# Kernel tuning notes

Hardware: AMD Instinct MI355X
Metric: run time of the kernel (lower is better)

Reference implementation:

```python
import jax, jax.numpy as jnp
import numpy as np


def setup_inputs() -> dict:
    key = jax.random.key(0)
    k1, k2, k3, k4, k5 = jax.random.split(key, 5)
    B, S, H, V = 16, 256, 1024, 32000
    std = 0.02
    return {
        "input_ids": jax.random.randint(k1, (B, S), 0, V, dtype=jnp.int64),
        "emb": jax.random.normal(k2, (V, H), dtype=jnp.float32) * std,
        "w_hx": jax.random.normal(k3, (H, H), dtype=jnp.float32) * std,
        "w_hh": jax.random.normal(k4, (H, H), dtype=jnp.float32) * std,
        "w_yh": jax.random.normal(k5, (V, H), dtype=jnp.float32) * std,
    }


def reference(input_ids, emb, w_hx, w_hh, w_yh):
    # input_ids: [B, S] int; emb: [V, H]; w_*: torch Linear weights [out, in]
    B, S = input_ids.shape
    H = emb.shape[1]
    x = emb[input_ids]                         # [B, S, H]
    # Precompute input contribution for all timesteps: x_t @ w_hx.T
    xin = jnp.einsum('bsh,oh->bso', x, w_hx)   # [B, S, H]
    h0 = jnp.zeros((B, H), dtype=x.dtype)

    def step(h, xin_t):
        h_new = jnp.tanh(xin_t + h @ w_hh.T)   # [B, H]
        return h_new, h_new

    _, hs = jax.lax.scan(step, h0, jnp.swapaxes(xin, 0, 1))  # hs: [S, B, H]
    hs = jnp.swapaxes(hs, 0, 1)                # [B, S, H]
    logits = jnp.einsum('bsh,vh->bsv', hs, w_yh)  # [B, S, V]
    return logits
```

## Files before the change

kernel.cpp:

```cpp
#include <hip/hip_runtime.h>
#include <stdint.h>

typedef __attribute__((ext_vector_type(8)))  short   short8;
typedef __attribute__((ext_vector_type(8)))  unsigned short ushort8;
typedef __attribute__((ext_vector_type(8)))  __bf16  bf16x8;
typedef __attribute__((ext_vector_type(4)))  float   floatx4;
typedef __attribute__((ext_vector_type(4)))  unsigned short ushort4v;

#define AS1 __attribute__((address_space(1)))
#define AS3 __attribute__((address_space(3)))

__device__ __forceinline__ unsigned short f2bf(float f) {
  unsigned u = __builtin_bit_cast(unsigned, f);
  u = (u + 0x7FFFu + ((u >> 16) & 1u)) >> 16;
  return (unsigned short)u;
}
__device__ __forceinline__ float bf2f(unsigned short h) {
  unsigned u = ((unsigned)h) << 16;
  return __builtin_bit_cast(float, u);
}

__global__ __launch_bounds__(256) void convert_bf16(const float* __restrict__ src,
                                                    unsigned short* __restrict__ dst,
                                                    int n) {
  int i = (blockIdx.x * 256 + threadIdx.x) * 4;
  if (i >= n) return;
  float4 v = *(const float4*)(src + i);
  ushort4v o;
  o.x = f2bf(v.x); o.y = f2bf(v.y); o.z = f2bf(v.z); o.w = f2bf(v.w);
  *(ushort4v*)(dst + i) = o;
}

__global__ __launch_bounds__(256) void detect_i64(const int* __restrict__ idbuf,
                                                  int* __restrict__ flag) {
  int v = 0;
  for (int i = threadIdx.x; i < 2048; i += 256) v |= idbuf[2 * i + 1];
  if (v != 0) atomicOr(flag, 1);
}

__global__ __launch_bounds__(256) void gather_embed(const int* __restrict__ ids,
                                                    const float* __restrict__ emb,
                                                    unsigned short* __restrict__ xbf,
                                                    const int* __restrict__ flag) {
  int i = blockIdx.x;
  int row = (*flag != 0) ? ids[i] : ids[2 * i];
  const float* src = emb + (size_t)row * 1024 + threadIdx.x * 4;
  float4 v = *(const float4*)src;
  ushort4v o;
  o.x = f2bf(v.x); o.y = f2bf(v.y); o.z = f2bf(v.z); o.w = f2bf(v.w);
  *(ushort4v*)(xbf + (size_t)i * 1024 + threadIdx.x * 4) = o;
}

__global__ __launch_bounds__(256) void gemm_bt(const unsigned short* __restrict__ A,
                                               const unsigned short* __restrict__ B,
                                               float* __restrict__ C,
                                               int M, int N, int K) {
  __shared__ unsigned short lA[128 * 64];
  __shared__ unsigned short lB[128 * 64];
  const int nwg  = gridDim.x;
  const int wgid = blockIdx.x;
  const int q    = nwg >> 3;
  const int swz  = (wgid & 7) * q + (wgid >> 3);
  const int ntx  = N >> 7;
  const int bx   = swz % ntx;
  const int by   = swz / ntx;
  const int tid  = threadIdx.x;
  const int lane = tid & 63;
  const int w    = tid >> 6;
  const int wr   = w >> 1, wc = w & 1;

  floatx4 acc[4][4];
#pragma unroll
  for (int m = 0; m < 4; ++m)
#pragma unroll
    for (int n = 0; n < 4; ++n) acc[m][n] = (floatx4){0.f, 0.f, 0.f, 0.f};

  const size_t rowA0 = (size_t)by * 128;
  const size_t colB0 = (size_t)bx * 128;

  for (int k0 = 0; k0 < K; k0 += 64) {
#pragma unroll
    for (int p = 0; p < 4; ++p) {
      int cc = p * 256 + tid;
      int r  = cc >> 3;
      int c8 = cc & 7;
      const unsigned short* srcA = A + (rowA0 + r) * K + k0 + c8 * 8;
      const unsigned short* srcB = B + (colB0 + r) * K + k0 + c8 * 8;
      __builtin_amdgcn_global_load_lds((const AS1 unsigned int*)srcA,
                                       (AS3 unsigned int*)&lA[cc * 8], 16, 0, 0);
      __builtin_amdgcn_global_load_lds((const AS1 unsigned int*)srcB,
                                       (AS3 unsigned int*)&lB[cc * 8], 16, 0, 0);
    }
    __syncthreads();
#pragma unroll
    for (int kk = 0; kk < 2; ++kk) {
      const int kofs = kk * 32 + (lane >> 4) * 8;
      bf16x8 af[4], bfv[4];
#pragma unroll
      for (int m = 0; m < 4; ++m) {
        int r = wr * 64 + m * 16 + (lane & 15);
        af[m] = *(const bf16x8*)&lA[r * 64 + kofs];
      }
#pragma unroll
      for (int n = 0; n < 4; ++n) {
        int r = wc * 64 + n * 16 + (lane & 15);
        bfv[n] = *(const bf16x8*)&lB[r * 64 + kofs];
      }
#pragma unroll
      for (int m = 0; m < 4; ++m)
#pragma unroll
        for (int n = 0; n < 4; ++n)
          acc[m][n] = __builtin_amdgcn_mfma_f32_16x16x32_bf16(af[m], bfv[n], acc[m][n], 0, 0, 0);
    }
    __syncthreads();
  }

#pragma unroll
  for (int m = 0; m < 4; ++m) {
#pragma unroll
    for (int j = 0; j < 4; ++j) {
      size_t row = rowA0 + wr * 64 + m * 16 + ((lane >> 4) * 4 + j);
      float* crow = C + row * (size_t)N + colB0 + wc * 64 + (lane & 15);
#pragma unroll
      for (int n = 0; n < 4; ++n) crow[n * 16] = acc[m][n][j];
    }
  }
}

__global__ __launch_bounds__(1024, 4) void rnn_step_all(const float* __restrict__ xin,
                                                        const unsigned short* __restrict__ whh_bf,
                                                        float* __restrict__ hs,
                                                        unsigned short* __restrict__ hs_bf) {
  const int b     = blockIdx.x >> 4;
  const int slice = blockIdx.x & 15;
  const int tid   = threadIdx.x;
  const int o     = tid & 63;
  const int kc    = tid >> 6;

  __shared__ __align__(16) float hl[1024];
  __shared__ float red[2][1024];

  float wf[64];
  {
    const unsigned short* wrow = whh_bf + (size_t)(slice * 64 + o) * 1024 + kc * 64;
#pragma unroll
    for (int j = 0; j < 8; ++j) {
      ushort8 wv = *(const ushort8*)(wrow + j * 8);
#pragma unroll
      for (int e = 0; e < 8; ++e) wf[j * 8 + e] = bf2f(wv[e]);
    }
#pragma unroll
    for (int j = 0; j < 64; ++j) asm volatile("" : "+v"(wf[j]));
  }

  const size_t bbase = (size_t)b * 256 * 1024;

  for (int t = 0; t < 256; ++t) {
    float s = 0.0f;
    if (tid < 64) s = xin[bbase + (size_t)t * 1024 + slice * 64 + tid];

    if (t == 0) {
      hl[tid] = 0.0f;
    } else {
      const float* src = &hs[bbase + (size_t)(t - 1) * 1024 + (size_t)kc * 64 + o];
      float v;
      do {
        v = __hip_atomic_load(src, __ATOMIC_RELAXED, __HIP_MEMORY_SCOPE_AGENT);
      } while (__any(v != v));
      hl[tid] = v;
    }

    float sum = 0.0f;
#pragma unroll
    for (int j4 = 0; j4 < 16; ++j4) {
      float4 hv = *(const float4*)&hl[kc * 64 + j4 * 4];
      sum += wf[j4 * 4 + 0] * hv.x + wf[j4 * 4 + 1] * hv.y +
             wf[j4 * 4 + 2] * hv.z + wf[j4 * 4 + 3] * hv.w;
    }
    red[t & 1][tid] = sum;
    __syncthreads();

    if (tid < 64) {
#pragma unroll
      for (int k2 = 0; k2 < 16; ++k2) s += red[t & 1][k2 * 64 + tid];
      float e  = __expf(2.0f * s);
      float hv = 1.0f - 2.0f * __builtin_amdgcn_rcpf(e + 1.0f);
      size_t idx = bbase + (size_t)t * 1024 + (size_t)slice * 64 + tid;
      __hip_atomic_store(&hs[idx], hv, __ATOMIC_RELAXED, __HIP_MEMORY_SCOPE_AGENT);
      hs_bf[idx] = f2bf(hv);
    }
  }
}

extern "C" void kernel_launch(void* const* d_in, const int* in_sizes, int n_in,
                              void* d_out, int out_size, void* d_ws, size_t ws_size,
                              hipStream_t stream) {
  const int*   ids  = (const int*)d_in[0];
  const float* emb  = (const float*)d_in[1];
  const float* w_hx = (const float*)d_in[2];
  const float* w_hh = (const float*)d_in[3];
  const float* w_yh = (const float*)d_in[4];
  float*       out  = (float*)d_out;

  const int B = 16, S = 256, H = 1024, V = 32000;
  const int BS = B * S;

  char*  ws  = (char*)d_ws;
  size_t off = 0;
  auto alloc = [&](size_t bytes) {
    size_t cur = off;
    off += (bytes + 255) & ~(size_t)255;
    return (void*)(ws + cur);
  };

  unsigned short* whx_bf = (unsigned short*)alloc((size_t)H * H * 2);
  unsigned short* whh_bf = (unsigned short*)alloc((size_t)H * H * 2);
  unsigned short* wyh_bf = (unsigned short*)alloc((size_t)V * H * 2);
  unsigned short* x_bf   = (unsigned short*)alloc((size_t)BS * H * 2);
  float*          xin    = (float*)alloc((size_t)BS * H * 4);
  float*          hs     = (float*)alloc((size_t)BS * H * 4);
  unsigned short* hs_bf  = (unsigned short*)alloc((size_t)BS * H * 2);
  int*            dflag  = (int*)alloc(256);

  hipMemsetAsync(hs, 0xFF, (size_t)BS * H * 4, stream);
  hipMemsetAsync(dflag, 0, 256, stream);

  detect_i64<<<dim3(1), dim3(256), 0, stream>>>(ids, dflag);
  convert_bf16<<<dim3((H * H) / 1024), dim3(256), 0, stream>>>(w_hx, whx_bf, H * H);
  convert_bf16<<<dim3((H * H) / 1024), dim3(256), 0, stream>>>(w_hh, whh_bf, H * H);
  convert_bf16<<<dim3((V * H) / 1024), dim3(256), 0, stream>>>(w_yh, wyh_bf, V * H);
  gather_embed<<<dim3(BS), dim3(256), 0, stream>>>(ids, emb, x_bf, dflag);

  gemm_bt<<<dim3((BS / 128) * (H / 128)), dim3(256), 0, stream>>>(x_bf, whx_bf, xin, BS, H, H);

  rnn_step_all<<<dim3(256), dim3(1024), 0, stream>>>(xin, whh_bf, hs, hs_bf);

  gemm_bt<<<dim3((BS / 128) * (V / 128)), dim3(256), 0, stream>>>(hs_bf, wyh_bf, out, BS, V, H);
}
```

Baseline: 931.9 us.

## Halve RNN block size and replace __syncthreads with LDS flag handoff

The recurrent step kernel now uses 512 threads per block, each holding 128 weights in registers instead of 64, which halves the cross-wave reduction. The per-step __syncthreads is replaced by per-wave LDS flags that only the reducing wave spins on, so the other waves can move on to poll the next timestep. This aims to cut barrier and reduction latency on the serial critical path. In exchange it doubles per-thread register use, and it relies on hand-placed waitcnt and sched_barrier ordering for correctness, which could race if the compiler reorders memory operations.

New measurement: 977.9 us. 1.05x slower.

```diff
diff --git a/kernel.cpp b/kernel.cpp
--- a/kernel.cpp
+++ b/kernel.cpp
@@ -127,10 +127,10 @@
   }
 }
 
-__global__ __launch_bounds__(1024, 4) void rnn_step_all(const float* __restrict__ xin,
-                                                        const unsigned short* __restrict__ whh_bf,
-                                                        float* __restrict__ hs,
-                                                        unsigned short* __restrict__ hs_bf) {
+__global__ __launch_bounds__(512, 2) void rnn_step_all(const float* __restrict__ xin,
+                                                       const unsigned short* __restrict__ whh_bf,
+                                                       float* __restrict__ hs,
+                                                       unsigned short* __restrict__ hs_bf) {
   const int b     = blockIdx.x >> 4;
   const int slice = blockIdx.x & 15;
   const int tid   = threadIdx.x;
@@ -138,54 +138,72 @@
   const int kc    = tid >> 6;
 
   __shared__ __align__(16) float hl[1024];
-  __shared__ float red[2][1024];
-
-  float wf[64];
+  __shared__ float red[2][512];
+  __shared__ unsigned lflag[2][8];
+
+  if (tid < 16) lflag[tid >> 3][tid & 7] = 0;
+  __syncthreads();
+
+  float wf[128];
   {
-    const unsigned short* wrow = whh_bf + (size_t)(slice * 64 + o) * 1024 + kc * 64;
-#pragma unroll
-    for (int j = 0; j < 8; ++j) {
+    const unsigned short* wrow = whh_bf + (size_t)(slice * 64 + o) * 1024 + kc * 128;
+#pragma unroll
+    for (int j = 0; j < 16; ++j) {
       ushort8 wv = *(const ushort8*)(wrow + j * 8);
 #pragma unroll
       for (int e = 0; e < 8; ++e) wf[j * 8 + e] = bf2f(wv[e]);
     }
 #pragma unroll
-    for (int j = 0; j < 64; ++j) asm volatile("" : "+v"(wf[j]));
+    for (int j = 0; j < 128; ++j) asm volatile("" : "+v"(wf[j]));
   }
 
   const size_t bbase = (size_t)b * 256 * 1024;
 
   for (int t = 0; t < 256; ++t) {
     float s = 0.0f;
-    if (tid < 64) s = xin[bbase + (size_t)t * 1024 + slice * 64 + tid];
+    if (tid < 64) s = xin[bbase + (size_t)t * 1024 + slice * 64 + o];
 
     if (t == 0) {
-      hl[tid] = 0.0f;
+      hl[kc * 128 + o]      = 0.0f;
+      hl[kc * 128 + 64 + o] = 0.0f;
     } else {
-      const float* src = &hs[bbase + (size_t)(t - 1) * 1024 + (size_t)kc * 64 + o];
-      float v;
+      const float* src = &hs[bbase + (size_t)(t - 1) * 1024 + (size_t)kc * 128];
+      float v1, v2;
       do {
-        v = __hip_atomic_load(src, __ATOMIC_RELAXED, __HIP_MEMORY_SCOPE_AGENT);
-      } while (__any(v != v));
-      hl[tid] = v;
-    }
-
-    float sum = 0.0f;
-#pragma unroll
-    for (int j4 = 0; j4 < 16; ++j4) {
-      float4 hv = *(const float4*)&hl[kc * 64 + j4 * 4];
-      sum += wf[j4 * 4 + 0] * hv.x + wf[j4 * 4 + 1] * hv.y +
-             wf[j4 * 4 + 2] * hv.z + wf[j4 * 4 + 3] * hv.w;
-    }
-    red[t & 1][tid] = sum;
-    __syncthreads();
+        v1 = __hip_atomic_load(src + o,      __ATOMIC_RELAXED, __HIP_MEMORY_SCOPE_AGENT);
+        v2 = __hip_atomic_load(src + 64 + o, __ATOMIC_RELAXED, __HIP_MEMORY_SCOPE_AGENT);
+      } while (__any((v1 != v1) | (v2 != v2)));
+      hl[kc * 128 + o]      = v1;
+      hl[kc * 128 + 64 + o] = v2;
+    }
+
+    float a0 = 0.f, a1 = 0.f, a2 = 0.f, a3 = 0.f;
+#pragma unroll
+    for (int j4 = 0; j4 < 32; ++j4) {
+      float4 hv = *(const float4*)&hl[kc * 128 + j4 * 4];
+      a0 += wf[j4 * 4 + 0] * hv.x; a1 += wf[j4 * 4 + 1] * hv.y;
+      a2 += wf[j4 * 4 + 2] * hv.z; a3 += wf[j4 * 4 + 3] * hv.w;
+    }
+    red[t & 1][tid] = (a0 + a1) + (a2 + a3);
+    asm volatile("s_waitcnt lgkmcnt(0)" ::: "memory");
+    __builtin_amdgcn_sched_barrier(0);
+    if (o == 0) lflag[t & 1][kc] = (unsigned)(t + 1);
 
     if (tid < 64) {
-#pragma unroll
-      for (int k2 = 0; k2 < 16; ++k2) s += red[t & 1][k2 * 64 + tid];
+      const volatile unsigned* fl = &lflag[t & 1][0];
+      bool rdy;
+      do {
+        rdy = true;
+#pragma unroll
+        for (int k = 0; k < 8; ++k) rdy = rdy && (fl[k] >= (unsigned)(t + 1));
+      } while (!rdy);
+      __builtin_amdgcn_sched_barrier(0);
+      asm volatile("" ::: "memory");
+#pragma unroll
+      for (int k2 = 0; k2 < 8; ++k2) s += red[t & 1][k2 * 64 + o];
       float e  = __expf(2.0f * s);
       float hv = 1.0f - 2.0f * __builtin_amdgcn_rcpf(e + 1.0f);
-      size_t idx = bbase + (size_t)t * 1024 + (size_t)slice * 64 + tid;
+      size_t idx = bbase + (size_t)t * 1024 + (size_t)slice * 64 + o;
       __hip_atomic_store(&hs[idx], hv, __ATOMIC_RELAXED, __HIP_MEMORY_SCOPE_AGENT);
       hs_bf[idx] = f2bf(hv);
     }
@@ -233,7 +251,7 @@
 
   gemm_bt<<<dim3((BS / 128) * (H / 128)), dim3(256), 0, stream>>>(x_bf, whx_bf, xin, BS, H, H);
 
-  rnn_step_all<<<dim3(256), dim3(1024), 0, stream>>>(xin, whh_bf, hs, hs_bf);
+  rnn_step_all<<<dim3(256), dim3(512), 0, stream>>>(xin, whh_bf, hs, hs_bf);
 
   gemm_bt<<<dim3((BS / 128) * (V / 128)), dim3(256), 0, stream>>>(hs_bf, wyh_bf, out, BS, V, H);
 }
```

## Replace per-batch scalar RNN recurrence with MFMA wavefronts over all batches

Applied to the files above, without the earlier changes.

The recurrent step moves from 256 blocks of 1024 threads (one per batch-slice) doing scalar FMAs with LDS reductions to 64 single-wave blocks. Each block owns 16 output neurons across all 16 batches and computes h@W_hh^T with bf16 MFMA, keeping its weights in registers. The hidden state now lives only in a time-major bf16 buffer that is polled with NaN sentinels, replacing the separate fp32 and bf16 copies. The GEMMs gain a row remap so xin is written time-major and logits are read back into batch-major order. This cuts per-step sync and reduction overhead and memory traffic, at the cost of bf16 rounding of the recurrent state and busy-wait spins on fewer waves.

Measured after the change: 1.845 ms. 98.0% more time.

```diff
diff --git a/kernel.cpp b/kernel.cpp
--- a/kernel.cpp
+++ b/kernel.cpp
@@ -14,10 +14,6 @@
   unsigned u = __builtin_bit_cast(unsigned, f);
   u = (u + 0x7FFFu + ((u >> 16) & 1u)) >> 16;
   return (unsigned short)u;
-}
-__device__ __forceinline__ float bf2f(unsigned short h) {
-  unsigned u = ((unsigned)h) << 16;
-  return __builtin_bit_cast(float, u);
 }
 
 __global__ __launch_bounds__(256) void convert_bf16(const float* __restrict__ src,
@@ -54,7 +50,7 @@
 __global__ __launch_bounds__(256) void gemm_bt(const unsigned short* __restrict__ A,
                                                const unsigned short* __restrict__ B,
                                                float* __restrict__ C,
-                                               int M, int N, int K) {
+                                               int M, int N, int K, int rowmap) {
   __shared__ unsigned short lA[128 * 64];
   __shared__ unsigned short lB[128 * 64];
   const int nwg  = gridDim.x;
@@ -120,75 +116,83 @@
 #pragma unroll
     for (int j = 0; j < 4; ++j) {
       size_t row = rowA0 + wr * 64 + m * 16 + ((lane >> 4) * 4 + j);
-      float* crow = C + row * (size_t)N + colB0 + wc * 64 + (lane & 15);
+      size_t orow = (rowmap == 0) ? row
+                  : (rowmap == 1) ? ((row & 255) * 16 + (row >> 8))
+                                  : ((row & 15) * 256 + (row >> 4));
+      float* crow = C + orow * (size_t)N + colB0 + wc * 64 + (lane & 15);
 #pragma unroll
       for (int n = 0; n < 4; ++n) crow[n * 16] = acc[m][n][j];
     }
   }
 }
 
-__global__ __launch_bounds__(1024, 4) void rnn_step_all(const float* __restrict__ xin,
-                                                        const unsigned short* __restrict__ whh_bf,
-                                                        float* __restrict__ hs,
-                                                        unsigned short* __restrict__ hs_bf) {
-  const int b     = blockIdx.x >> 4;
-  const int slice = blockIdx.x & 15;
-  const int tid   = threadIdx.x;
-  const int o     = tid & 63;
-  const int kc    = tid >> 6;
-
-  __shared__ __align__(16) float hl[1024];
-  __shared__ float red[2][1024];
-
-  float wf[64];
-  {
-    const unsigned short* wrow = whh_bf + (size_t)(slice * 64 + o) * 1024 + kc * 64;
-#pragma unroll
-    for (int j = 0; j < 8; ++j) {
-      ushort8 wv = *(const ushort8*)(wrow + j * 8);
-#pragma unroll
-      for (int e = 0; e < 8; ++e) wf[j * 8 + e] = bf2f(wv[e]);
-    }
-#pragma unroll
-    for (int j = 0; j < 64; ++j) asm volatile("" : "+v"(wf[j]));
-  }
-
-  const size_t bbase = (size_t)b * 256 * 1024;
+__global__ __launch_bounds__(64, 1) void rnn_mfma(const float* __restrict__ xin,
+                                                  const unsigned short* __restrict__ whh,
+                                                  unsigned short* __restrict__ hst) {
+  const int lane = threadIdx.x;
+  const int n    = lane & 15;
+  const int g    = lane >> 4;
+  const int out_base = blockIdx.x * 16;
+
+  bf16x8 wb[32];
+#pragma unroll
+  for (int ks = 0; ks < 32; ++ks)
+    wb[ks] = *(const bf16x8*)&whh[(size_t)(out_base + n) * 1024 + g * 8 + ks * 32];
 
   for (int t = 0; t < 256; ++t) {
-    float s = 0.0f;
-    if (tid < 64) s = xin[bbase + (size_t)t * 1024 + slice * 64 + tid];
-
-    if (t == 0) {
-      hl[tid] = 0.0f;
-    } else {
-      const float* src = &hs[bbase + (size_t)(t - 1) * 1024 + (size_t)kc * 64 + o];
-      float v;
-      do {
-        v = __hip_atomic_load(src, __ATOMIC_RELAXED, __HIP_MEMORY_SCOPE_AGENT);
-      } while (__any(v != v));
-      hl[tid] = v;
-    }
-
-    float sum = 0.0f;
-#pragma unroll
-    for (int j4 = 0; j4 < 16; ++j4) {
-      float4 hv = *(const float4*)&hl[kc * 64 + j4 * 4];
-      sum += wf[j4 * 4 + 0] * hv.x + wf[j4 * 4 + 1] * hv.y +
-             wf[j4 * 4 + 2] * hv.z + wf[j4 * 4 + 3] * hv.w;
-    }
-    red[t & 1][tid] = sum;
-    __syncthreads();
-
-    if (tid < 64) {
-#pragma unroll
-      for (int k2 = 0; k2 < 16; ++k2) s += red[t & 1][k2 * 64 + tid];
-      float e  = __expf(2.0f * s);
-      float hv = 1.0f - 2.0f * __builtin_amdgcn_rcpf(e + 1.0f);
-      size_t idx = bbase + (size_t)t * 1024 + (size_t)slice * 64 + tid;
-      __hip_atomic_store(&hs[idx], hv, __ATOMIC_RELAXED, __HIP_MEMORY_SCOPE_AGENT);
-      hs_bf[idx] = f2bf(hv);
-    }
+    float xi[4];
+#pragma unroll
+    for (int jj = 0; jj < 4; ++jj)
+      xi[jj] = xin[(size_t)(t * 16 + g * 4 + jj) * 1024 + out_base + n];
+
+    floatx4 s4 = (floatx4){0.f, 0.f, 0.f, 0.f};
+    if (t > 0) {
+      const unsigned long long* src = (const unsigned long long*)
+          &hst[(size_t)(t - 1) * 16384 + (size_t)n * 1024 + g * 8];
+      for (;;) {
+        unsigned long long lo[32], hi[32];
+#pragma unroll
+        for (int ks = 0; ks < 32; ++ks) {
+          lo[ks] = __hip_atomic_load(src + ks * 8 + 0, __ATOMIC_RELAXED, __HIP_MEMORY_SCOPE_AGENT);
+          hi[ks] = __hip_atomic_load(src + ks * 8 + 1, __ATOMIC_RELAXED, __HIP_MEMORY_SCOPE_AGENT);
+        }
+        floatx4 a0 = (floatx4){0,0,0,0}, a1 = (floatx4){0,0,0,0};
+        floatx4 a2 = (floatx4){0,0,0,0}, a3 = (floatx4){0,0,0,0};
+#pragma unroll
+        for (int ks = 0; ks < 32; ++ks) {
+          bf16x8 af = __builtin_bit_cast(bf16x8, (ulonglong2){lo[ks], hi[ks]});
+          if      ((ks & 3) == 0) a0 = __builtin_amdgcn_mfma_f32_16x16x32_bf16(af, wb[ks], a0, 0, 0, 0);
+          else if ((ks & 3) == 1) a1 = __builtin_amdgcn_mfma_f32_16x16x32_bf16(af, wb[ks], a1, 0, 0, 0);
+          else if ((ks & 3) == 2) a2 = __builtin_amdgcn_mfma_f32_16x16x32_bf16(af, wb[ks], a2, 0, 0, 0);
+          else                    a3 = __builtin_amdgcn_mfma_f32_16x16x32_bf16(af, wb[ks], a3, 0, 0, 0);
+        }
+        s4 = (a0 + a1) + (a2 + a3);
+        int bad = __builtin_isnan(s4[0]) | __builtin_isnan(s4[1]) |
+                  __builtin_isnan(s4[2]) | __builtin_isnan(s4[3]);
+        if (!__any(bad)) break;
+      }
+    }
+
+    float hv[4];
+#pragma unroll
+    for (int jj = 0; jj < 4; ++jj) {
+      float s = s4[jj] + xi[jj];
+      float e = __expf(2.0f * s);
+      hv[jj] = 1.0f - 2.0f * __builtin_amdgcn_rcpf(e + 1.0f);
+    }
+    float pv[4];
+#pragma unroll
+    for (int jj = 0; jj < 4; ++jj) pv[jj] = __shfl_xor(hv[jj], 1);
+    const int ev = (lane & 1) == 0;
+    const int jA = ev ? 0 : 2, jB = ev ? 1 : 3;
+    unsigned dA = ev ? ((unsigned)f2bf(hv[jA]) | ((unsigned)f2bf(pv[jA]) << 16))
+                     : ((unsigned)f2bf(pv[jA]) | ((unsigned)f2bf(hv[jA]) << 16));
+    unsigned dB = ev ? ((unsigned)f2bf(hv[jB]) | ((unsigned)f2bf(pv[jB]) << 16))
+                     : ((unsigned)f2bf(pv[jB]) | ((unsigned)f2bf(hv[jB]) << 16));
+    unsigned* rowA = (unsigned*)&hst[(size_t)t * 16384 + (size_t)(g * 4 + jA) * 1024 + out_base + (n & ~1)];
+    unsigned* rowB = (unsigned*)&hst[(size_t)t * 16384 + (size_t)(g * 4 + jB) * 1024 + out_base + (n & ~1)];
+    __hip_atomic_store(rowA, dA, __ATOMIC_RELAXED, __HIP_MEMORY_SCOPE_AGENT);
+    __hip_atomic_store(rowB, dB, __ATOMIC_RELAXED, __HIP_MEMORY_SCOPE_AGENT);
   }
 }
 
@@ -218,11 +222,10 @@
   unsigned short* wyh_bf = (unsigned short*)alloc((size_t)V * H * 2);
   unsigned short* x_bf   = (unsigned short*)alloc((size_t)BS * H * 2);
   float*          xin    = (float*)alloc((size_t)BS * H * 4);
-  float*          hs     = (float*)alloc((size_t)BS * H * 4);
-  unsigned short* hs_bf  = (unsigned short*)alloc((size_t)BS * H * 2);
+  unsigned short* hst    = (unsigned short*)alloc((size_t)BS * H * 2);
   int*            dflag  = (int*)alloc(256);
 
-  hipMemsetAsync(hs, 0xFF, (size_t)BS * H * 4, stream);
+  hipMemsetAsync(hst, 0xFF, (size_t)BS * H * 2, stream);
   hipMemsetAsync(dflag, 0, 256, stream);
 
   detect_i64<<<dim3(1), dim3(256), 0, stream>>>(ids, dflag);
@@ -231,9 +234,9 @@
   convert_bf16<<<dim3((V * H) / 1024), dim3(256), 0, stream>>>(w_yh, wyh_bf, V * H);
   gather_embed<<<dim3(BS), dim3(256), 0, stream>>>(ids, emb, x_bf, dflag);
 
-  gemm_bt<<<dim3((BS / 128) * (H / 128)), dim3(256), 0, stream>>>(x_bf, whx_bf, xin, BS, H, H);
-
-  rnn_step_all<<<dim3(256), dim3(1024), 0, stream>>>(xin, whh_bf, hs, hs_bf);
-
-  gemm_bt<<<dim3((BS / 128) * (V / 128)), dim3(256), 0, stream>>>(hs_bf, wyh_bf, out, BS, V, H);
-}
+  gemm_bt<<<dim3((BS / 128) * (H / 128)), dim3(256), 0, stream>>>(x_bf, whx_bf, xin, BS, H, H, 1);
+
+  rnn_mfma<<<dim3(64), dim3(64), 0, stream>>>(xin, whh_bf, hst);
+
+  gemm_bt<<<dim3((BS / 128) * (V / 128)), dim3(256), 0, stream>>>(hst, wyh_bf, out, BS, V, H, 2);
+}
```
